# Optimization experiments

Hardware: AMD Instinct MI355X
Metric: run time of the kernel (lower is better)

The kernel has to match this reference:

```python
import jax, jax.numpy as jnp
import numpy as np

B, T, C = 4, 2048, 768
NH = 12
HD = C // NH  # 64


def setup_inputs() -> dict:
    key = jax.random.key(0)
    k1, k2, k3 = jax.random.split(key, 3)
    x = jax.random.normal(k1, (B, T, C), dtype=jnp.float32)
    W_attn = jax.random.normal(k2, (C, 3 * C), dtype=jnp.float32) * (1.0 / np.sqrt(C))
    b_attn = jnp.zeros((3 * C,), dtype=jnp.float32)
    W_proj = jax.random.normal(k3, (C, C), dtype=jnp.float32) * (1.0 / np.sqrt(C))
    b_proj = jnp.zeros((C,), dtype=jnp.float32)
    return {"x": x, "W_attn": W_attn, "b_attn": b_attn, "W_proj": W_proj, "b_proj": b_proj}


def reference(x, W_attn, b_attn, W_proj, b_proj):
    b, t, c = x.shape
    nh, hd = NH, c // NH
    qkv = x @ W_attn + b_attn                      # (B,T,3C)
    q, k, v = jnp.split(qkv, 3, axis=2)
    # (B,T,C) -> (B,NH,T,HD)
    q = q.reshape(b, t, nh, hd).transpose(0, 2, 1, 3)
    k = k.reshape(b, t, nh, hd).transpose(0, 2, 1, 3)
    v = v.reshape(b, t, nh, hd).transpose(0, 2, 1, 3)
    att = jnp.einsum('bhqd,bhkd->bhqk', q, k) / jnp.sqrt(jnp.float32(hd))
    causal = jnp.tril(jnp.ones((t, t), dtype=bool))
    att = jnp.where(causal, att, -jnp.inf)
    att = jax.nn.softmax(att, axis=-1)
    y = jnp.einsum('bhqk,bhkd->bhqd', att, v)      # (B,NH,T,HD)
    y = y.transpose(0, 2, 1, 3).reshape(b, t, c)
    return y @ W_proj + b_proj
```

## Files before the change

kernel.cpp:

```cpp
#include <hip/hip_runtime.h>
#include <hip/hip_bf16.h>
#include <cstdint>

typedef __bf16 bf16;
typedef __bf16 bf16x4 __attribute__((ext_vector_type(4)));
typedef __bf16 bf16x8 __attribute__((ext_vector_type(8)));
typedef float f32x4 __attribute__((ext_vector_type(4)));

#define B_  4
#define T_  2048
#define C_  768
#define NH_ 12
#define HD_ 64
#define BH_ (B_ * NH_)

__device__ __forceinline__ f32x4 mfma16(bf16x8 a, bf16x8 b, f32x4 c) {
  return __builtin_amdgcn_mfma_f32_16x16x32_bf16(a, b, c, 0, 0, 0);
}

__device__ __forceinline__ void gload16(const bf16* src, bf16* dst) {
  __builtin_amdgcn_global_load_lds(
      (const __attribute__((address_space(1))) unsigned int*)src,
      (__attribute__((address_space(3))) unsigned int*)dst, 16, 0, 0);
}

__global__ __launch_bounds__(256) void cvt_kernel(const float* __restrict__ in,
                                                  bf16* __restrict__ out, int n4) {
  int i = blockIdx.x * blockDim.x + threadIdx.x;
  if (i < n4) {
    float4 v = reinterpret_cast<const float4*>(in)[i];
    bf16x4 o;
    o[0] = (bf16)v.x; o[1] = (bf16)v.y; o[2] = (bf16)v.z; o[3] = (bf16)v.w;
    reinterpret_cast<bf16x4*>(out)[i] = o;
  }
}

__global__ __launch_bounds__(256) void wtr_kernel(const float* __restrict__ W,
                                                  bf16* __restrict__ WT, int K, int N) {
  __shared__ bf16 t[64][72];
  const int tid = threadIdx.x;
  const int k0 = blockIdx.x * 64, n0 = blockIdx.y * 64;
  {
    const int r = tid >> 2, cg = (tid & 3) * 16;
    const float* src = W + (size_t)(k0 + r) * N + n0 + cg;
    float4 a0 = reinterpret_cast<const float4*>(src)[0];
    float4 a1 = reinterpret_cast<const float4*>(src)[1];
    float4 a2 = reinterpret_cast<const float4*>(src)[2];
    float4 a3 = reinterpret_cast<const float4*>(src)[3];
    bf16x8 lo, hi;
    lo[0]=(bf16)a0.x; lo[1]=(bf16)a0.y; lo[2]=(bf16)a0.z; lo[3]=(bf16)a0.w;
    lo[4]=(bf16)a1.x; lo[5]=(bf16)a1.y; lo[6]=(bf16)a1.z; lo[7]=(bf16)a1.w;
    hi[0]=(bf16)a2.x; hi[1]=(bf16)a2.y; hi[2]=(bf16)a2.z; hi[3]=(bf16)a2.w;
    hi[4]=(bf16)a3.x; hi[5]=(bf16)a3.y; hi[6]=(bf16)a3.z; hi[7]=(bf16)a3.w;
    *reinterpret_cast<bf16x8*>(&t[r][cg]) = lo;
    *reinterpret_cast<bf16x8*>(&t[r][cg + 8]) = hi;
  }
  __syncthreads();
  {
    const int n = tid & 63, kg = (tid >> 6) * 16;
    bf16x8 o0, o1;
#pragma unroll
    for (int i = 0; i < 8; ++i) { o0[i] = t[kg + i][n]; o1[i] = t[kg + 8 + i][n]; }
    bf16* dst = WT + (size_t)(n0 + n) * K + k0 + kg;
    *reinterpret_cast<bf16x8*>(dst) = o0;
    *reinterpret_cast<bf16x8*>(dst + 8) = o1;
  }
}

template <int EPI>
__global__ __launch_bounds__(256) void gemm_mfma(
    const bf16* __restrict__ A, const bf16* __restrict__ BT,
    const float* __restrict__ bias, int M, int N, int K,
    bf16* __restrict__ q, bf16* __restrict__ k_, bf16* __restrict__ v,
    float* __restrict__ out) {
  __shared__ bf16 AlF[128 * 32];
  __shared__ bf16 BlF[128 * 32];

  const int tid = threadIdx.x;
  const int wid = tid >> 6, lane = tid & 63;
  unsigned orig = blockIdx.y * gridDim.x + blockIdx.x;
  unsigned cpx = (gridDim.x * gridDim.y) >> 3;
  unsigned work = (orig & 7) * cpx + (orig >> 3);
  const int m0 = (work / gridDim.x) * 128, n0 = (work % gridDim.x) * 128;
  const int wm = (wid >> 1) * 64, wn = (wid & 1) * 64;
  const int r = lane & 15, g = lane >> 4;

  f32x4 acc[4][4] = {};

  const int srow = tid >> 2;
  const int scol = (tid & 3) * 8;

  for (int k0 = 0; k0 < K; k0 += 32) {
    __syncthreads();
#pragma unroll
    for (int c = 0; c < 2; ++c) {
      gload16(A  + (size_t)(m0 + c * 64 + srow) * K + k0 + scol, AlF + c * 2048 + wid * 512);
      gload16(BT + (size_t)(n0 + c * 64 + srow) * K + k0 + scol, BlF + c * 2048 + wid * 512);
    }
    __syncthreads();

    bf16x8 af[4], bfr[4];
#pragma unroll
    for (int fm = 0; fm < 4; ++fm)
      af[fm] = *reinterpret_cast<bf16x8*>(&AlF[(wm + fm * 16 + r) * 32 + g * 8]);
#pragma unroll
    for (int fn = 0; fn < 4; ++fn)
      bfr[fn] = *reinterpret_cast<bf16x8*>(&BlF[(wn + fn * 16 + r) * 32 + g * 8]);
#pragma unroll
    for (int fm = 0; fm < 4; ++fm)
#pragma unroll
      for (int fn = 0; fn < 4; ++fn)
        acc[fm][fn] = mfma16(af[fm], bfr[fn], acc[fm][fn]);
  }

#pragma unroll
  for (int fm = 0; fm < 4; ++fm)
#pragma unroll
    for (int fn = 0; fn < 4; ++fn)
#pragma unroll
      for (int j = 0; j < 4; ++j) {
        int m = m0 + wm + fm * 16 + g * 4 + j;
        int n = n0 + wn + fn * 16 + r;
        float val = acc[fm][fn][j] + bias[n];
        if (EPI == 0) {
          int b = m >> 11, t = m & 2047;
          bf16* dst; int c;
          if (n < 768)        { dst = q;  c = n;        val *= 0.180336881f; }
          else if (n < 1536)  { dst = k_; c = n - 768;  }
          else                { dst = v;  c = n - 1536; }
          int h = c >> 6, d = c & 63;
          dst[(((size_t)(b * NH_ + h)) * T_ + t) * HD_ + d] = (bf16)val;
        } else {
          out[(size_t)m * N + n] = val;
        }
      }
}

__global__ __launch_bounds__(256) void attn_fwd(
    const bf16* __restrict__ Q, const bf16* __restrict__ K,
    const bf16* __restrict__ V, bf16* __restrict__ Y) {
  __shared__ bf16 Kl[64][72];
  __shared__ bf16 VtF[64 * 72];
  __shared__ bf16 Pl[4][16][72];

  const int tid = threadIdx.x;
  const int wid = tid >> 6, lane = tid & 63;
  const int r = lane & 15, g = lane >> 4;

  unsigned orig = blockIdx.y * 16 + blockIdx.x;
  unsigned work = (orig & 7) * 96 + (orig >> 3);
  const int bx = work & 15;
  const int bh = work >> 4;
  const int bidx = bh / NH_, h = bh % NH_;

  const bf16* Qb = Q + (size_t)bh * T_ * HD_;
  const bf16* Kb = K + (size_t)bh * T_ * HD_;
  const bf16* Vb = V + (size_t)bh * T_ * HD_;

  const int krow = tid >> 3;
  const int kc8 = (tid & 7) * 8;

#pragma unroll
  for (int pass = 0; pass < 2; ++pass) {
    const int tile = pass ? 31 - bx : bx;
    const int qt0 = tile * 64 + wid * 16;

    bf16x8 qf[2];
#pragma unroll
    for (int kc = 0; kc < 2; ++kc)
      qf[kc] = *reinterpret_cast<const bf16x8*>(
          Qb + (size_t)(qt0 + r) * HD_ + kc * 32 + g * 8);

    float m_st = -INFINITY;
    float l_p = 0.f;
    f32x4 o[4] = {};

    const int nsteps = tile + 1;
    for (int s = 0; s < nsteps; ++s) {
      const int kv0 = s * 64;
      __syncthreads();
#pragma unroll
      for (int p = 0; p < 2; ++p) {
        int row = p * 32 + krow;
        bf16x8 kv8 = *reinterpret_cast<const bf16x8*>(Kb + (size_t)(kv0 + row) * HD_ + kc8);
        *reinterpret_cast<bf16x8*>(&Kl[row][kc8]) = kv8;
        bf16x8 vv8 = *reinterpret_cast<const bf16x8*>(Vb + (size_t)(kv0 + row) * HD_ + kc8);
        int xorb = (((row >> 3) ^ (tid & 7)) << 3) + (row & 7);
#pragma unroll
        for (int j = 0; j < 8; ++j) VtF[(kc8 + j) * 72 + xorb] = vv8[j];
      }
      __syncthreads();

      f32x4 s4[4] = {};
      __builtin_amdgcn_s_setprio(1);
#pragma unroll
      for (int cb = 0; cb < 4; ++cb)
#pragma unroll
        for (int kc = 0; kc < 2; ++kc) {
          bf16x8 kf = *reinterpret_cast<bf16x8*>(&Kl[cb * 16 + r][kc * 32 + g * 8]);
          s4[cb] = mfma16(kf, qf[kc], s4[cb]);
        }
      __builtin_amdgcn_s_setprio(0);

      if (s == tile) {
#pragma unroll
        for (int cb = 0; cb < 4; ++cb)
#pragma unroll
          for (int j = 0; j < 4; ++j)
            if (kv0 + cb * 16 + g * 4 + j > qt0 + r) s4[cb][j] = -INFINITY;
      }

      float pmax = fmaxf(
          fmaxf(fmaxf(fmaxf(s4[0][0], s4[0][1]), fmaxf(s4[0][2], s4[0][3])),
                fmaxf(fmaxf(s4[1][0], s4[1][1]), fmaxf(s4[1][2], s4[1][3]))),
          fmaxf(fmaxf(fmaxf(s4[2][0], s4[2][1]), fmaxf(s4[2][2], s4[2][3])),
                fmaxf(fmaxf(s4[3][0], s4[3][1]), fmaxf(s4[3][2], s4[3][3]))));
      pmax = fmaxf(pmax, __shfl_xor(pmax, 16));
      pmax = fmaxf(pmax, __shfl_xor(pmax, 32));

      if (!__all(pmax - m_st <= 8.0f)) {
        float sc = exp2f(m_st - pmax);
        m_st = pmax;
        l_p *= sc;
        float sc0 = __shfl(sc, g * 4 + 0);
        float sc1 = __shfl(sc, g * 4 + 1);
        float sc2 = __shfl(sc, g * 4 + 2);
        float sc3 = __shfl(sc, g * 4 + 3);
#pragma unroll
        for (int dn = 0; dn < 4; ++dn) {
          o[dn][0] *= sc0; o[dn][1] *= sc1; o[dn][2] *= sc2; o[dn][3] *= sc3;
        }
      }

      float sum = 0.f;
#pragma unroll
      for (int cb = 0; cb < 4; ++cb) {
        bf16x4 pw;
#pragma unroll
        for (int j = 0; j < 4; ++j) {
          float pv = exp2f(s4[cb][j] - m_st);
          sum += pv;
          pw[j] = (bf16)pv;
        }
        *reinterpret_cast<bf16x4*>(&Pl[wid][r][cb * 16 + g * 4]) = pw;
      }
      l_p += sum;

      __builtin_amdgcn_s_setprio(1);
#pragma unroll
      for (int kc = 0; kc < 2; ++kc) {
        bf16x8 pf = *reinterpret_cast<bf16x8*>(&Pl[wid][r][kc * 32 + g * 8]);
#pragma unroll
        for (int dn = 0; dn < 4; ++dn) {
          int d = dn * 16 + r;
          bf16x8 vf = *reinterpret_cast<bf16x8*>(
              &VtF[d * 72 + (((4 * kc + g) ^ (d >> 3)) << 3)]);
          o[dn] = mfma16(pf, vf, o[dn]);
        }
      }
      __builtin_amdgcn_s_setprio(0);
    }

    l_p += __shfl_xor(l_p, 16);
    l_p += __shfl_xor(l_p, 32);
    float linv = 1.f / l_p;
    float i0 = __shfl(linv, g * 4 + 0);
    float i1 = __shfl(linv, g * 4 + 1);
    float i2 = __shfl(linv, g * 4 + 2);
    float i3 = __shfl(linv, g * 4 + 3);

#pragma unroll
    for (int j = 0; j < 4; ++j) {
      float inv = j == 0 ? i0 : (j == 1 ? i1 : (j == 2 ? i2 : i3));
      int qrow = qt0 + g * 4 + j;
#pragma unroll
      for (int dn = 0; dn < 4; ++dn) {
        int d = dn * 16 + r;
        Y[((size_t)bidx * T_ + qrow) * C_ + h * HD_ + d] = (bf16)(o[dn][j] * inv);
      }
    }
  }
}

extern "C" void kernel_launch(void* const* d_in, const int* in_sizes, int n_in,
                              void* d_out, int out_size, void* d_ws, size_t ws_size,
                              hipStream_t stream) {
  const float* x  = (const float*)d_in[0];
  const float* Wa = (const float*)d_in[1];
  const float* ba = (const float*)d_in[2];
  const float* Wp = (const float*)d_in[3];
  const float* bp = (const float*)d_in[4];
  float* out = (float*)d_out;

  char* ws = (char*)d_ws;
  size_t off = 0;
  auto alloc = [&](size_t bytes) {
    char* p = ws + off;
    off += (bytes + 255) & ~(size_t)255;
    return p;
  };
  bf16* xb   = (bf16*)alloc((size_t)B_ * T_ * C_ * 2);
  bf16* WaT  = (bf16*)alloc((size_t)C_ * 3 * C_ * 2);
  bf16* WpT  = (bf16*)alloc((size_t)C_ * C_ * 2);
  bf16* Qb   = (bf16*)alloc((size_t)BH_ * T_ * HD_ * 2);
  bf16* Kb   = (bf16*)alloc((size_t)BH_ * T_ * HD_ * 2);
  bf16* Vb   = (bf16*)alloc((size_t)BH_ * T_ * HD_ * 2);
  bf16* Yb   = (bf16*)alloc((size_t)B_ * T_ * C_ * 2);

  const int M = B_ * T_;

  cvt_kernel<<<(M * C_ / 4) / 256, 256, 0, stream>>>(x, xb, M * C_ / 4);
  wtr_kernel<<<dim3(C_ / 64, 3 * C_ / 64), 256, 0, stream>>>(Wa, WaT, C_, 3 * C_);
  wtr_kernel<<<dim3(C_ / 64, C_ / 64), 256, 0, stream>>>(Wp, WpT, C_, C_);

  gemm_mfma<0><<<dim3(3 * C_ / 128, M / 128), 256, 0, stream>>>(
      xb, WaT, ba, M, 3 * C_, C_, Qb, Kb, Vb, nullptr);

  attn_fwd<<<dim3(16, BH_), 256, 0, stream>>>(Qb, Kb, Vb, Yb);

  gemm_mfma<1><<<dim3(C_ / 128, M / 128), 256, 0, stream>>>(
      Yb, WpT, bp, M, C_, C_, nullptr, nullptr, nullptr, out);
}
```

Measured before the change: 244.1 us.

## Fuse attention causal passes over shared KV loads and deepen GEMM K-tile to 64

```diff
diff --git a/kernel.cpp b/kernel.cpp
--- a/kernel.cpp
+++ b/kernel.cpp
@@ -73,8 +73,8 @@
     const float* __restrict__ bias, int M, int N, int K,
     bf16* __restrict__ q, bf16* __restrict__ k_, bf16* __restrict__ v,
     float* __restrict__ out) {
-  __shared__ bf16 AlF[128 * 32];
-  __shared__ bf16 BlF[128 * 32];
+  __shared__ bf16 AlF[128 * 64];
+  __shared__ bf16 BlF[128 * 64];
 
   const int tid = threadIdx.x;
   const int wid = tid >> 6, lane = tid & 63;
@@ -87,30 +87,33 @@
 
   f32x4 acc[4][4] = {};
 
-  const int srow = tid >> 2;
-  const int scol = (tid & 3) * 8;
-
-  for (int k0 = 0; k0 < K; k0 += 32) {
+  const int l8 = lane >> 3;
+  const int c8 = (lane & 7) * 8;
+
+  for (int k0 = 0; k0 < K; k0 += 64) {
     __syncthreads();
 #pragma unroll
-    for (int c = 0; c < 2; ++c) {
-      gload16(A  + (size_t)(m0 + c * 64 + srow) * K + k0 + scol, AlF + c * 2048 + wid * 512);
-      gload16(BT + (size_t)(n0 + c * 64 + srow) * K + k0 + scol, BlF + c * 2048 + wid * 512);
+    for (int i = 0; i < 4; ++i) {
+      int row = i * 32 + wid * 8 + l8;
+      gload16(A  + (size_t)(m0 + row) * K + k0 + c8, AlF + (i * 32 + wid * 8) * 64);
+      gload16(BT + (size_t)(n0 + row) * K + k0 + c8, BlF + (i * 32 + wid * 8) * 64);
     }
     __syncthreads();
 
-    bf16x8 af[4], bfr[4];
-#pragma unroll
-    for (int fm = 0; fm < 4; ++fm)
-      af[fm] = *reinterpret_cast<bf16x8*>(&AlF[(wm + fm * 16 + r) * 32 + g * 8]);
-#pragma unroll
-    for (int fn = 0; fn < 4; ++fn)
-      bfr[fn] = *reinterpret_cast<bf16x8*>(&BlF[(wn + fn * 16 + r) * 32 + g * 8]);
-#pragma unroll
-    for (int fm = 0; fm < 4; ++fm)
+#pragma unroll
+    for (int kc = 0; kc < 2; ++kc) {
+      bf16x8 bfr[4];
 #pragma unroll
       for (int fn = 0; fn < 4; ++fn)
-        acc[fm][fn] = mfma16(af[fm], bfr[fn], acc[fm][fn]);
+        bfr[fn] = *reinterpret_cast<bf16x8*>(&BlF[(wn + fn * 16 + r) * 64 + kc * 32 + g * 8]);
+#pragma unroll
+      for (int fm = 0; fm < 4; ++fm) {
+        bf16x8 af = *reinterpret_cast<bf16x8*>(&AlF[(wm + fm * 16 + r) * 64 + kc * 32 + g * 8]);
+#pragma unroll
+        for (int fn = 0; fn < 4; ++fn)
+          acc[fm][fn] = mfma16(af, bfr[fn], acc[fm][fn]);
+      }
+    }
   }
 
 #pragma unroll
@@ -141,7 +144,7 @@
     const bf16* __restrict__ V, bf16* __restrict__ Y) {
   __shared__ bf16 Kl[64][72];
   __shared__ bf16 VtF[64 * 72];
-  __shared__ bf16 Pl[4][16][72];
+  __shared__ bf16 Pl[4][2][16][72];
 
   const int tid = threadIdx.x;
   const int wid = tid >> 6, lane = tid & 63;
@@ -160,37 +163,38 @@
   const int krow = tid >> 3;
   const int kc8 = (tid & 7) * 8;
 
-#pragma unroll
-  for (int pass = 0; pass < 2; ++pass) {
-    const int tile = pass ? 31 - bx : bx;
-    const int qt0 = tile * 64 + wid * 16;
-
-    bf16x8 qf[2];
-#pragma unroll
-    for (int kc = 0; kc < 2; ++kc)
-      qf[kc] = *reinterpret_cast<const bf16x8*>(
-          Qb + (size_t)(qt0 + r) * HD_ + kc * 32 + g * 8);
-
-    float m_st = -INFINITY;
-    float l_p = 0.f;
-    f32x4 o[4] = {};
-
-    const int nsteps = tile + 1;
-    for (int s = 0; s < nsteps; ++s) {
-      const int kv0 = s * 64;
-      __syncthreads();
-#pragma unroll
-      for (int p = 0; p < 2; ++p) {
-        int row = p * 32 + krow;
-        bf16x8 kv8 = *reinterpret_cast<const bf16x8*>(Kb + (size_t)(kv0 + row) * HD_ + kc8);
-        *reinterpret_cast<bf16x8*>(&Kl[row][kc8]) = kv8;
-        bf16x8 vv8 = *reinterpret_cast<const bf16x8*>(Vb + (size_t)(kv0 + row) * HD_ + kc8);
-        int xorb = (((row >> 3) ^ (tid & 7)) << 3) + (row & 7);
-#pragma unroll
-        for (int j = 0; j < 8; ++j) VtF[(kc8 + j) * 72 + xorb] = vv8[j];
-      }
-      __syncthreads();
-
+  const int tA = bx, tB = 31 - bx;
+  const int qt0A = tA * 64 + wid * 16;
+  const int qt0B = tB * 64 + wid * 16;
+
+  bf16x8 qfA[2], qfB[2];
+#pragma unroll
+  for (int kc = 0; kc < 2; ++kc) {
+    qfA[kc] = *reinterpret_cast<const bf16x8*>(Qb + (size_t)(qt0A + r) * HD_ + kc * 32 + g * 8);
+    qfB[kc] = *reinterpret_cast<const bf16x8*>(Qb + (size_t)(qt0B + r) * HD_ + kc * 32 + g * 8);
+  }
+
+  float mA = -INFINITY, lA = 0.f, mB = -INFINITY, lB = 0.f;
+  f32x4 oA[4] = {}, oB[4] = {};
+
+  const int nsteps = tB + 1;
+  for (int s = 0; s < nsteps; ++s) {
+    const int kv0 = s * 64;
+    __syncthreads();
+#pragma unroll
+    for (int p = 0; p < 2; ++p) {
+      int row = p * 32 + krow;
+      bf16x8 kv8 = *reinterpret_cast<const bf16x8*>(Kb + (size_t)(kv0 + row) * HD_ + kc8);
+      *reinterpret_cast<bf16x8*>(&Kl[row][kc8]) = kv8;
+      bf16x8 vv8 = *reinterpret_cast<const bf16x8*>(Vb + (size_t)(kv0 + row) * HD_ + kc8);
+      int xorb = (((row >> 3) ^ (tid & 7)) << 3) + (row & 7);
+#pragma unroll
+      for (int j = 0; j < 8; ++j) VtF[(kc8 + j) * 72 + xorb] = vv8[j];
+    }
+    __syncthreads();
+
+    auto process = [&](const bf16x8 (&qf)[2], float& m_st, float& l_p, f32x4 (&o)[4],
+                       bf16* PlW, int qt0, bool diag) {
       f32x4 s4[4] = {};
       __builtin_amdgcn_s_setprio(1);
 #pragma unroll
@@ -202,7 +206,7 @@
         }
       __builtin_amdgcn_s_setprio(0);
 
-      if (s == tile) {
+      if (diag) {
 #pragma unroll
         for (int cb = 0; cb < 4; ++cb)
 #pragma unroll
@@ -242,14 +246,14 @@
           sum += pv;
           pw[j] = (bf16)pv;
         }
-        *reinterpret_cast<bf16x4*>(&Pl[wid][r][cb * 16 + g * 4]) = pw;
+        *reinterpret_cast<bf16x4*>(&PlW[r * 72 + cb * 16 + g * 4]) = pw;
       }
       l_p += sum;
 
       __builtin_amdgcn_s_setprio(1);
 #pragma unroll
       for (int kc = 0; kc < 2; ++kc) {
-        bf16x8 pf = *reinterpret_cast<bf16x8*>(&Pl[wid][r][kc * 32 + g * 8]);
+        bf16x8 pf = *reinterpret_cast<bf16x8*>(&PlW[r * 72 + kc * 32 + g * 8]);
 #pragma unroll
         for (int dn = 0; dn < 4; ++dn) {
           int d = dn * 16 + r;
@@ -259,8 +263,14 @@
         }
       }
       __builtin_amdgcn_s_setprio(0);
-    }
-
+    };
+
+    process(qfB, mB, lB, oB, &Pl[wid][1][0][0], qt0B, s == tB);
+    if (s <= tA)
+      process(qfA, mA, lA, oA, &Pl[wid][0][0][0], qt0A, s == tA);
+  }
+
+  auto epi = [&](float l_p, f32x4 (&o)[4], int qt0) {
     l_p += __shfl_xor(l_p, 16);
     l_p += __shfl_xor(l_p, 32);
     float linv = 1.f / l_p;
@@ -268,7 +278,6 @@
     float i1 = __shfl(linv, g * 4 + 1);
     float i2 = __shfl(linv, g * 4 + 2);
     float i3 = __shfl(linv, g * 4 + 3);
-
 #pragma unroll
     for (int j = 0; j < 4; ++j) {
       float inv = j == 0 ? i0 : (j == 1 ? i1 : (j == 2 ? i2 : i3));
@@ -279,7 +288,9 @@
         Y[((size_t)bidx * T_ + qrow) * C_ + h * HD_ + d] = (bf16)(o[dn][j] * inv);
       }
     }
-  }
+  };
+  epi(lA, oA, qt0A);
+  epi(lB, oB, qt0B);
 }
 
 extern "C" void kernel_launch(void* const* d_in, const int* in_sizes, int n_in,
```

Result: slower. 265.9 us (+8.9%).

## Deepen GEMM K-tile to 64 and register-prefetch next K/V tile in attention

Applied to the files above, without the earlier changes.

```diff
diff --git a/kernel.cpp b/kernel.cpp
--- a/kernel.cpp
+++ b/kernel.cpp
@@ -73,8 +73,8 @@
     const float* __restrict__ bias, int M, int N, int K,
     bf16* __restrict__ q, bf16* __restrict__ k_, bf16* __restrict__ v,
     float* __restrict__ out) {
-  __shared__ bf16 AlF[128 * 32];
-  __shared__ bf16 BlF[128 * 32];
+  __shared__ bf16 AlF[128 * 64];
+  __shared__ bf16 BlF[128 * 64];
 
   const int tid = threadIdx.x;
   const int wid = tid >> 6, lane = tid & 63;
@@ -87,30 +87,33 @@
 
   f32x4 acc[4][4] = {};
 
-  const int srow = tid >> 2;
-  const int scol = (tid & 3) * 8;
-
-  for (int k0 = 0; k0 < K; k0 += 32) {
+  const int l8 = lane >> 3;
+  const int c8 = (lane & 7) * 8;
+
+  for (int k0 = 0; k0 < K; k0 += 64) {
     __syncthreads();
 #pragma unroll
-    for (int c = 0; c < 2; ++c) {
-      gload16(A  + (size_t)(m0 + c * 64 + srow) * K + k0 + scol, AlF + c * 2048 + wid * 512);
-      gload16(BT + (size_t)(n0 + c * 64 + srow) * K + k0 + scol, BlF + c * 2048 + wid * 512);
+    for (int i = 0; i < 4; ++i) {
+      int row = i * 32 + wid * 8 + l8;
+      gload16(A  + (size_t)(m0 + row) * K + k0 + c8, AlF + (i * 32 + wid * 8) * 64);
+      gload16(BT + (size_t)(n0 + row) * K + k0 + c8, BlF + (i * 32 + wid * 8) * 64);
     }
     __syncthreads();
 
-    bf16x8 af[4], bfr[4];
-#pragma unroll
-    for (int fm = 0; fm < 4; ++fm)
-      af[fm] = *reinterpret_cast<bf16x8*>(&AlF[(wm + fm * 16 + r) * 32 + g * 8]);
-#pragma unroll
-    for (int fn = 0; fn < 4; ++fn)
-      bfr[fn] = *reinterpret_cast<bf16x8*>(&BlF[(wn + fn * 16 + r) * 32 + g * 8]);
-#pragma unroll
-    for (int fm = 0; fm < 4; ++fm)
+#pragma unroll
+    for (int kc = 0; kc < 2; ++kc) {
+      bf16x8 bfr[4];
 #pragma unroll
       for (int fn = 0; fn < 4; ++fn)
-        acc[fm][fn] = mfma16(af[fm], bfr[fn], acc[fm][fn]);
+        bfr[fn] = *reinterpret_cast<bf16x8*>(&BlF[(wn + fn * 16 + r) * 64 + kc * 32 + g * 8]);
+#pragma unroll
+      for (int fm = 0; fm < 4; ++fm) {
+        bf16x8 af = *reinterpret_cast<bf16x8*>(&AlF[(wm + fm * 16 + r) * 64 + kc * 32 + g * 8]);
+#pragma unroll
+        for (int fn = 0; fn < 4; ++fn)
+          acc[fm][fn] = mfma16(af, bfr[fn], acc[fm][fn]);
+      }
+    }
   }
 
 #pragma unroll
@@ -176,20 +179,36 @@
     f32x4 o[4] = {};
 
     const int nsteps = tile + 1;
+
+    bf16x8 kreg[2], vreg[2];
+#pragma unroll
+    for (int p = 0; p < 2; ++p) {
+      int row = p * 32 + krow;
+      kreg[p] = *reinterpret_cast<const bf16x8*>(Kb + (size_t)row * HD_ + kc8);
+      vreg[p] = *reinterpret_cast<const bf16x8*>(Vb + (size_t)row * HD_ + kc8);
+    }
+
     for (int s = 0; s < nsteps; ++s) {
       const int kv0 = s * 64;
-      __syncthreads();
 #pragma unroll
       for (int p = 0; p < 2; ++p) {
         int row = p * 32 + krow;
-        bf16x8 kv8 = *reinterpret_cast<const bf16x8*>(Kb + (size_t)(kv0 + row) * HD_ + kc8);
-        *reinterpret_cast<bf16x8*>(&Kl[row][kc8]) = kv8;
-        bf16x8 vv8 = *reinterpret_cast<const bf16x8*>(Vb + (size_t)(kv0 + row) * HD_ + kc8);
+        *reinterpret_cast<bf16x8*>(&Kl[row][kc8]) = kreg[p];
         int xorb = (((row >> 3) ^ (tid & 7)) << 3) + (row & 7);
 #pragma unroll
-        for (int j = 0; j < 8; ++j) VtF[(kc8 + j) * 72 + xorb] = vv8[j];
+        for (int j = 0; j < 8; ++j) VtF[(kc8 + j) * 72 + xorb] = vreg[p][j];
       }
       __syncthreads();
+
+      if (s + 1 < nsteps) {
+        const int kvn = kv0 + 64;
+#pragma unroll
+        for (int p = 0; p < 2; ++p) {
+          int row = kvn + p * 32 + krow;
+          kreg[p] = *reinterpret_cast<const bf16x8*>(Kb + (size_t)row * HD_ + kc8);
+          vreg[p] = *reinterpret_cast<const bf16x8*>(Vb + (size_t)row * HD_ + kc8);
+        }
+      }
 
       f32x4 s4[4] = {};
       __builtin_amdgcn_s_setprio(1);
@@ -259,6 +278,7 @@
         }
       }
       __builtin_amdgcn_s_setprio(0);
+      __syncthreads();
     }
 
     l_p += __shfl_xor(l_p, 16);
```

After: 241.6 us. No clear change (-1.0%).
